# Performance work log

Measured on AMD Instinct MI355X. Metric: run time of the kernel, lower is better.

Reference implementation:

```python
import jax, jax.numpy as jnp
import numpy as np

THRESHOLD = 0.1
EPS = 1e-05


def setup_inputs() -> dict:
    key = jax.random.key(0)
    kx, kl, k1, k2 = jax.random.split(key, 4)
    B, S, D = 8, 4096, 1024
    Dh = max(2, D // 2)
    x = jax.random.normal(kx, (B, S, D), dtype=jnp.float32)
    # trailing (right) padding with random valid lengths in [S//2, S]
    lengths = jax.random.randint(kl, (B,), S // 2, S + 1)
    pad = jnp.arange(S)[None, :] >= lengths[:, None]  # [B, S] bool, True = padded
    W1 = jax.random.normal(k1, (D, Dh), dtype=jnp.float32) * (1.0 / np.sqrt(D))
    b1 = jnp.zeros((Dh,), dtype=jnp.float32)
    W2 = jax.random.normal(k2, (Dh, 1), dtype=jnp.float32) * (1.0 / np.sqrt(Dh))
    b2 = jnp.zeros((1,), dtype=jnp.float32)
    return {"x": x, "pad": pad, "W1": W1, "b1": b1, "W2": W2, "b2": b2}


def reference(x, pad, W1, b1, W2, b2):
    B, S, D = x.shape
    pos = jnp.arange(S)
    # number of valid (non-pad) tokens per batch; pad is trailing
    length = S - jnp.sum(pad, axis=1)  # [B]

    # tiny gate MLP: Linear -> ReLU -> Linear, squashed to (0, 1)
    h = jax.nn.relu(jnp.einsum('bsd,dh->bsh', x, W1) + b1)
    y = jnp.einsum('bsh,ho->bso', h, W2) + b2          # [B, S, 1]
    y = (1.0 + jnp.tanh(10.0 * y)) * 0.5

    # zero out gate values at padded positions (torch loop: y[i, n:] = 0)
    valid = pos[None, :] < length[:, None]             # [B, S]
    y = jnp.where(valid[..., None], y, 0.0)

    # lift so at least one token passes the threshold
    adjust = jnp.clip(EPS + THRESHOLD - jnp.max(y, axis=1), 0.0)  # [B, 1]
    y = y + adjust[:, None, :]                         # broadcast over seq

    u = x * y                                          # gated features [B, S, D]
    ys = y[..., 0]                                     # [B, S]
    u_mask = (ys > THRESHOLD) & (~pad)                 # tokens kept
    new_len = jnp.sum(u_mask, axis=1)                  # [B]

    # compact kept tokens to the front of each row (stable sort: kept first,
    # original order preserved) -- the mask-scatter v[v_mask] = u[u_mask]
    order = jnp.argsort(~u_mask, axis=1, stable=True)  # [B, S]
    v = jnp.take_along_axis(u, order[..., None], axis=1)
    v_mask = pos[None, :] < new_len[:, None]           # [B, S]
    v = jnp.where(v_mask[..., None], v, 0.0)
    v_pad = ~v_mask
    return v, v_pad
```

## Files before the change

### kernel.cpp

```cpp
#include <hip/hip_runtime.h>
#include <math.h>

#define NB 8
#define NS 4096
#define ND 1024
#define NDH 512
#define NTOK (NB*NS)
#define THRESH 0.1f
#define EPSV 1e-5f

using short8   = __attribute__((ext_vector_type(8)))  short;
using floatx16 = __attribute__((ext_vector_type(16))) float;
using floatv4  = __attribute__((ext_vector_type(4)))  float;

__device__ __forceinline__ unsigned short f32_to_bf16_rne(float f) {
  union { float f; unsigned u; } v; v.f = f;
  unsigned r = v.u + 0x7fffu + ((v.u >> 16) & 1u);
  return (unsigned short)(r >> 16);
}
__device__ __forceinline__ float bf16_to_f32(unsigned short h) {
  union { unsigned u; float f; } v; v.u = ((unsigned)h) << 16;
  return v.f;
}

__global__ __launch_bounds__(256)
void k0_prep(const float* __restrict__ W1, unsigned short* __restrict__ Wf,
             unsigned int* __restrict__ rowmax) {
  __shared__ float sw[16][513];
  const int t = threadIdx.x;
  const int k16 = blockIdx.x;
  if (k16 == 0 && t < NB) rowmax[t] = 0u;
#pragma unroll
  for (int i = 0; i < 8; ++i) {
    int flat = i * 256 + t;
    int r = flat >> 7, c4 = (flat & 127) << 2;
    *(float4*)&sw[r][c4] = *(const float4*)(W1 + (size_t)(k16 * 16 + r) * NDH + c4);
  }
  __syncthreads();
#pragma unroll
  for (int q = 0; q < 4; ++q) {
    int ss = q * 256 + t;
    int n32 = ss >> 6, lane = ss & 63;
    int n = n32 * 32 + (lane & 31);
    int kb = (lane >> 5) * 8;
    unsigned hi2[4], lo2[4];
#pragma unroll
    for (int j = 0; j < 4; ++j) {
      float w0 = sw[kb + 2 * j][n], w1 = sw[kb + 2 * j + 1][n];
      unsigned short h0 = f32_to_bf16_rne(w0), h1 = f32_to_bf16_rne(w1);
      unsigned short l0 = f32_to_bf16_rne(w0 - bf16_to_f32(h0));
      unsigned short l1 = f32_to_bf16_rne(w1 - bf16_to_f32(h1));
      hi2[j] = (unsigned)h0 | ((unsigned)h1 << 16);
      lo2[j] = (unsigned)l0 | ((unsigned)l1 << 16);
    }
    size_t cb = ((size_t)(n32 * 64 + k16) * 2) * 512 + (size_t)lane * 8;
    *(uint4*)(Wf + cb)       = make_uint4(hi2[0], hi2[1], hi2[2], hi2[3]);
    *(uint4*)(Wf + cb + 512) = make_uint4(lo2[0], lo2[1], lo2[2], lo2[3]);
  }
}

__global__ __launch_bounds__(256, 2)
void k1_gemm(const float* __restrict__ x, const unsigned short* __restrict__ Wf,
             const float* __restrict__ b1, const float* __restrict__ W2,
             const int* __restrict__ pad, const float* __restrict__ b2,
             float* __restrict__ ysq, unsigned int* __restrict__ rowmax) {
  __shared__ __align__(16) unsigned short sx[2][2][64 * 72];
  __shared__ float red[4][64];

  const int tid = threadIdx.x;
  const int wave = tid >> 6, lane = tid & 63;
  const int l31 = lane & 31, h5 = lane >> 5;
  const int tok0 = blockIdx.x * 64;

  floatx16 acc[2][4];
#pragma unroll
  for (int mt = 0; mt < 2; ++mt)
#pragma unroll
    for (int nt = 0; nt < 4; ++nt)
#pragma unroll
      for (int r = 0; r < 16; ++r) acc[mt][nt][r] = 0.f;

  const int sm = tid >> 2;
  const int sk = (tid & 3) * 16;
  const float* xrow = x + (size_t)(tok0 + sm) * ND + sk;

  const unsigned short* wb[4];
#pragma unroll
  for (int nt = 0; nt < 4; ++nt)
    wb[nt] = Wf + (((size_t)(wave * 4 + nt) * 64) * 2) * 512 + (size_t)lane * 8;

  auto stage_cvt = [&](int bf, const float4& a0, const float4& a1,
                       const float4& a2, const float4& a3) {
    float v16[16] = {a0.x, a0.y, a0.z, a0.w, a1.x, a1.y, a1.z, a1.w,
                     a2.x, a2.y, a2.z, a2.w, a3.x, a3.y, a3.z, a3.w};
    unsigned hp[8], lp[8];
#pragma unroll
    for (int j = 0; j < 8; ++j) {
      unsigned short h0 = f32_to_bf16_rne(v16[2 * j]);
      unsigned short h1 = f32_to_bf16_rne(v16[2 * j + 1]);
      unsigned short l0 = f32_to_bf16_rne(v16[2 * j] - bf16_to_f32(h0));
      unsigned short l1 = f32_to_bf16_rne(v16[2 * j + 1] - bf16_to_f32(h1));
      hp[j] = (unsigned)h0 | ((unsigned)h1 << 16);
      lp[j] = (unsigned)l0 | ((unsigned)l1 << 16);
    }
    *(uint4*)&sx[bf][0][sm * 72 + sk]     = make_uint4(hp[0], hp[1], hp[2], hp[3]);
    *(uint4*)&sx[bf][0][sm * 72 + sk + 8] = make_uint4(hp[4], hp[5], hp[6], hp[7]);
    *(uint4*)&sx[bf][1][sm * 72 + sk]     = make_uint4(lp[0], lp[1], lp[2], lp[3]);
    *(uint4*)&sx[bf][1][sm * 72 + sk + 8] = make_uint4(lp[4], lp[5], lp[6], lp[7]);
  };

  {
    float4 a0 = *(const float4*)xrow;
    float4 a1 = *(const float4*)(xrow + 4);
    float4 a2 = *(const float4*)(xrow + 8);
    float4 a3 = *(const float4*)(xrow + 12);
    stage_cvt(0, a0, a1, a2, a3);
  }

  for (int it = 0; it < 16; ++it) {
    const int p = it & 1;
    __syncthreads();
    float4 pa0, pa1, pa2, pa3;
    if (it < 15) {
      const float* xp = xrow + (it + 1) * 64;
      pa0 = *(const float4*)xp;
      pa1 = *(const float4*)(xp + 4);
      pa2 = *(const float4*)(xp + 8);
      pa3 = *(const float4*)(xp + 12);
    }
#pragma unroll
    for (int kh = 0; kh < 4; ++kh) {
      short8 bh[4], bl[4];
#pragma unroll
      for (int nt = 0; nt < 4; ++nt) {
        const unsigned short* q = wb[nt] + ((size_t)(4 * it + kh) * 2) * 512;
        bh[nt] = *(const short8*)(q);
        bl[nt] = *(const short8*)(q + 512);
      }
      short8 ah[2], al[2];
#pragma unroll
      for (int mt = 0; mt < 2; ++mt) {
        ah[mt] = *(const short8*)&sx[p][0][(mt * 32 + l31) * 72 + kh * 16 + h5 * 8];
        al[mt] = *(const short8*)&sx[p][1][(mt * 32 + l31) * 72 + kh * 16 + h5 * 8];
      }
#pragma unroll
      for (int nt = 0; nt < 4; ++nt)
#pragma unroll
        for (int mt = 0; mt < 2; ++mt)
          acc[mt][nt] = __builtin_amdgcn_mfma_f32_32x32x16_bf16(ah[mt], bh[nt], acc[mt][nt], 0, 0, 0);
#pragma unroll
      for (int nt = 0; nt < 4; ++nt)
#pragma unroll
        for (int mt = 0; mt < 2; ++mt)
          acc[mt][nt] = __builtin_amdgcn_mfma_f32_32x32x16_bf16(al[mt], bh[nt], acc[mt][nt], 0, 0, 0);
#pragma unroll
      for (int nt = 0; nt < 4; ++nt)
#pragma unroll
        for (int mt = 0; mt < 2; ++mt)
          acc[mt][nt] = __builtin_amdgcn_mfma_f32_32x32x16_bf16(ah[mt], bl[nt], acc[mt][nt], 0, 0, 0);
    }
    if (it < 15) stage_cvt(p ^ 1, pa0, pa1, pa2, pa3);
  }

  float b1v[4], w2v[4];
#pragma unroll
  for (int nt = 0; nt < 4; ++nt) {
    const int n = wave * 128 + nt * 32 + l31;
    b1v[nt] = b1[n];
    w2v[nt] = W2[n];
  }
#pragma unroll
  for (int mt = 0; mt < 2; ++mt) {
    float pr[16];
#pragma unroll
    for (int r = 0; r < 16; ++r) pr[r] = 0.f;
#pragma unroll
    for (int nt = 0; nt < 4; ++nt)
#pragma unroll
      for (int r = 0; r < 16; ++r)
        pr[r] += fmaxf(acc[mt][nt][r] + b1v[nt], 0.f) * w2v[nt];
#pragma unroll
    for (int m = 1; m <= 16; m <<= 1)
#pragma unroll
      for (int r = 0; r < 16; ++r) pr[r] += __shfl_xor(pr[r], m, 64);
    if (l31 == 0) {
#pragma unroll
      for (int r = 0; r < 16; ++r) {
        int row = (r & 3) + 8 * (r >> 2) + 4 * h5;
        red[wave][mt * 32 + row] = pr[r];
      }
    }
  }
  __syncthreads();
  if (tid < 64) {
    float s = red[0][tid] + red[1][tid] + red[2][tid] + red[3][tid];
    const int t = tok0 + tid;
    float yl = s + b2[0];
    float y = (1.f + tanhf(10.f * yl)) * 0.5f;
    if (pad[t]) y = 0.f;
    ysq[t] = y;
    float m = y;
#pragma unroll
    for (int o = 32; o >= 1; o >>= 1) m = fmaxf(m, __shfl_xor(m, o, 64));
    if (tid == 0) atomicMax(rowmax + (t >> 12), __float_as_uint(m));
  }
}

__global__ __launch_bounds__(1024)
void k2b(const float* __restrict__ ysq, const int* __restrict__ pad,
         const unsigned int* __restrict__ rowmax, float* __restrict__ gval,
         int* __restrict__ src_of_dest, int* __restrict__ new_len,
         float* __restrict__ vpad_out) {
  __shared__ int ssum[16];
  const int b = blockIdx.x, tid = threadIdx.x;
  const int lane = tid & 63, wv = tid >> 6;
  const int base = b * NS, s0 = tid * 4;
  const float adj = fmaxf(EPSV + THRESH - __uint_as_float(rowmax[b]), 0.f);

  float4 yq = *(const float4*)(ysq + base + s0);
  int4 pq = *(const int4*)(pad + base + s0);
  float yv[4] = {yq.x + adj, yq.y + adj, yq.z + adj, yq.w + adj};
  int pv[4] = {pq.x, pq.y, pq.z, pq.w};
  unsigned km = 0;
  int cnt = 0;
#pragma unroll
  for (int i = 0; i < 4; ++i) {
    bool keep = (yv[i] > THRESH) && !pv[i];
    if (keep) { km |= (1u << i); ++cnt; }
  }
  int inc = cnt;
#pragma unroll
  for (int o = 1; o < 64; o <<= 1) {
    int tmp = __shfl_up(inc, o, 64);
    if (lane >= o) inc += tmp;
  }
  if (lane == 63) ssum[wv] = inc;
  __syncthreads();
  int wpre = 0;
  int total = 0;
#pragma unroll
  for (int w = 0; w < 16; ++w) {
    int sv = ssum[w];
    if (w < wv) wpre += sv;
    total += sv;
  }
  int off = wpre + inc - cnt;
#pragma unroll
  for (int i = 0; i < 4; ++i) {
    int s = s0 + i;
    if ((km >> i) & 1u) {
      src_of_dest[base + off] = s;
      gval[base + off] = yv[i];
      ++off;
    }
    vpad_out[base + s] = (s >= total) ? 1.f : 0.f;
  }
  if (tid == 0) new_len[b] = total;
}

__global__ __launch_bounds__(256)
void k3_gather(const float* __restrict__ x, const float* __restrict__ gval,
               const int* __restrict__ src_of_dest, const int* __restrict__ new_len,
               float* __restrict__ v) {
  const int slot0 = blockIdx.x * 16;
  const int b = slot0 >> 12;
  const int nl = new_len[b];
  const int tid = threadIdx.x;
#pragma unroll
  for (int i = 0; i < 16; ++i) {
    const int slot = slot0 + i;
    const int dest = slot & (NS - 1);
    floatv4* vo = (floatv4*)(v + (size_t)slot * ND);
    floatv4 r;
    if (dest < nl) {
      const int src = src_of_dest[slot];
      const float g = gval[slot];
      floatv4 xv = ((const floatv4*)(x + ((size_t)b * NS + src) * ND))[tid];
      r = xv * g;
    } else {
      r = (floatv4)(0.f);
    }
    __builtin_nontemporal_store(r, vo + tid);
  }
}

extern "C" void kernel_launch(void* const* d_in, const int* in_sizes, int n_in,
                              void* d_out, int out_size, void* d_ws, size_t ws_size,
                              hipStream_t stream) {
  const float* x   = (const float*)d_in[0];
  const int*   pad = (const int*)d_in[1];
  const float* W1  = (const float*)d_in[2];
  const float* b1  = (const float*)d_in[3];
  const float* W2  = (const float*)d_in[4];
  const float* b2  = (const float*)d_in[5];

  float* v    = (float*)d_out;
  float* vpad = v + (size_t)NTOK * ND;

  unsigned short* Wf = (unsigned short*)(v + 24000000);

  float* ysq  = (float*)d_ws;
  float* gval = ysq + NTOK;
  int* src    = (int*)(gval + NTOK);
  int* nlen   = src + NTOK;
  unsigned int* rowmax = (unsigned int*)(nlen + NB);

  k0_prep<<<64, 256, 0, stream>>>(W1, Wf, rowmax);
  k1_gemm<<<NTOK / 64, 256, 0, stream>>>(x, Wf, b1, W2, pad, b2, ysq, rowmax);
  k2b<<<NB, 1024, 0, stream>>>(ysq, pad, rowmax, gval, src, nlen, vpad);
  k3_gather<<<NTOK / 16, 256, 0, stream>>>(x, gval, src, nlen, v);
}
```

Measured before the change: 315.4 us.

## Fuse per-row scan/compaction into GEMM tail via last-block-done counter

Removes the separate k2b kernel. Each GEMM block now bumps a per-batch-row atomic counter, and the last block to finish a row computes the row max, the threshold mask, the prefix scan and the scatter indices. This saves one kernel launch and the reads of the per-row atomicMax. In exchange the tail work runs on a single 256-thread block per row with 16 tokens per thread, and it relies on a threadfence/counter pattern for correctness.

```diff
diff --git a/kernel.cpp b/kernel.cpp
--- a/kernel.cpp
+++ b/kernel.cpp
@@ -25,11 +25,11 @@
 
 __global__ __launch_bounds__(256)
 void k0_prep(const float* __restrict__ W1, unsigned short* __restrict__ Wf,
-             unsigned int* __restrict__ rowmax) {
+             int* __restrict__ done_cnt) {
   __shared__ float sw[16][513];
   const int t = threadIdx.x;
   const int k16 = blockIdx.x;
-  if (k16 == 0 && t < NB) rowmax[t] = 0u;
+  if (k16 == 0 && t < NB) done_cnt[t] = 0;
 #pragma unroll
   for (int i = 0; i < 8; ++i) {
     int flat = i * 256 + t;
@@ -63,9 +63,14 @@
 void k1_gemm(const float* __restrict__ x, const unsigned short* __restrict__ Wf,
              const float* __restrict__ b1, const float* __restrict__ W2,
              const int* __restrict__ pad, const float* __restrict__ b2,
-             float* __restrict__ ysq, unsigned int* __restrict__ rowmax) {
+             float* __restrict__ ysq, int* __restrict__ done_cnt,
+             float* __restrict__ gval, int* __restrict__ src_of_dest,
+             int* __restrict__ new_len, float* __restrict__ vpad) {
   __shared__ __align__(16) unsigned short sx[2][2][64 * 72];
   __shared__ float red[4][64];
+  __shared__ float smax[4];
+  __shared__ int ssum[4];
+  __shared__ int sflag;
 
   const int tid = threadIdx.x;
   const int wave = tid >> 6, lane = tid & 63;
@@ -199,63 +204,63 @@
     float y = (1.f + tanhf(10.f * yl)) * 0.5f;
     if (pad[t]) y = 0.f;
     ysq[t] = y;
-    float m = y;
+  }
+  __threadfence();
+  __syncthreads();
+  const int brow = tok0 >> 12;
+  if (tid == 0) {
+    int prev = atomicAdd(&done_cnt[brow], 1);
+    sflag = (prev == 63) ? 1 : 0;
+  }
+  __syncthreads();
+  if (sflag) {
+    __threadfence();
+    const int base = brow * NS, s0 = tid * 16;
+    const int wv = wave;
+    float yv[16];
+#pragma unroll
+    for (int i = 0; i < 16; ++i) yv[i] = ysq[base + s0 + i];
+    float m = 0.f;
+#pragma unroll
+    for (int i = 0; i < 16; ++i) m = fmaxf(m, yv[i]);
 #pragma unroll
     for (int o = 32; o >= 1; o >>= 1) m = fmaxf(m, __shfl_xor(m, o, 64));
-    if (tid == 0) atomicMax(rowmax + (t >> 12), __float_as_uint(m));
-  }
-}
-
-__global__ __launch_bounds__(1024)
-void k2b(const float* __restrict__ ysq, const int* __restrict__ pad,
-         const unsigned int* __restrict__ rowmax, float* __restrict__ gval,
-         int* __restrict__ src_of_dest, int* __restrict__ new_len,
-         float* __restrict__ vpad_out) {
-  __shared__ int ssum[16];
-  const int b = blockIdx.x, tid = threadIdx.x;
-  const int lane = tid & 63, wv = tid >> 6;
-  const int base = b * NS, s0 = tid * 4;
-  const float adj = fmaxf(EPSV + THRESH - __uint_as_float(rowmax[b]), 0.f);
-
-  float4 yq = *(const float4*)(ysq + base + s0);
-  int4 pq = *(const int4*)(pad + base + s0);
-  float yv[4] = {yq.x + adj, yq.y + adj, yq.z + adj, yq.w + adj};
-  int pv[4] = {pq.x, pq.y, pq.z, pq.w};
-  unsigned km = 0;
-  int cnt = 0;
-#pragma unroll
-  for (int i = 0; i < 4; ++i) {
-    bool keep = (yv[i] > THRESH) && !pv[i];
-    if (keep) { km |= (1u << i); ++cnt; }
-  }
-  int inc = cnt;
-#pragma unroll
-  for (int o = 1; o < 64; o <<= 1) {
-    int tmp = __shfl_up(inc, o, 64);
-    if (lane >= o) inc += tmp;
-  }
-  if (lane == 63) ssum[wv] = inc;
-  __syncthreads();
-  int wpre = 0;
-  int total = 0;
-#pragma unroll
-  for (int w = 0; w < 16; ++w) {
-    int sv = ssum[w];
-    if (w < wv) wpre += sv;
-    total += sv;
-  }
-  int off = wpre + inc - cnt;
-#pragma unroll
-  for (int i = 0; i < 4; ++i) {
-    int s = s0 + i;
-    if ((km >> i) & 1u) {
-      src_of_dest[base + off] = s;
-      gval[base + off] = yv[i];
-      ++off;
-    }
-    vpad_out[base + s] = (s >= total) ? 1.f : 0.f;
-  }
-  if (tid == 0) new_len[b] = total;
+    if (lane == 0) smax[wv] = m;
+    __syncthreads();
+    const float rmax = fmaxf(fmaxf(smax[0], smax[1]), fmaxf(smax[2], smax[3]));
+    const float adj = fmaxf(EPSV + THRESH - rmax, 0.f);
+    unsigned km = 0;
+    int cnt = 0;
+#pragma unroll
+    for (int i = 0; i < 16; ++i) {
+      yv[i] += adj;
+      bool keep = (yv[i] > THRESH) && !pad[base + s0 + i];
+      if (keep) { km |= (1u << i); ++cnt; }
+    }
+    int inc = cnt;
+#pragma unroll
+    for (int o = 1; o < 64; o <<= 1) {
+      int tmp = __shfl_up(inc, o, 64);
+      if (lane >= o) inc += tmp;
+    }
+    if (lane == 63) ssum[wv] = inc;
+    __syncthreads();
+    int wpre = 0;
+    for (int w = 0; w < wv; ++w) wpre += ssum[w];
+    const int total = ssum[0] + ssum[1] + ssum[2] + ssum[3];
+    int off = wpre + inc - cnt;
+#pragma unroll
+    for (int i = 0; i < 16; ++i) {
+      int sdx = s0 + i;
+      if ((km >> i) & 1u) {
+        src_of_dest[base + off] = sdx;
+        gval[base + off] = yv[i];
+        ++off;
+      }
+      vpad[base + sdx] = (sdx >= total) ? 1.f : 0.f;
+    }
+    if (tid == 0) new_len[brow] = total;
+  }
 }
 
 __global__ __launch_bounds__(256)
@@ -303,10 +308,10 @@
   float* gval = ysq + NTOK;
   int* src    = (int*)(gval + NTOK);
   int* nlen   = src + NTOK;
-  unsigned int* rowmax = (unsigned int*)(nlen + NB);
-
-  k0_prep<<<64, 256, 0, stream>>>(W1, Wf, rowmax);
-  k1_gemm<<<NTOK / 64, 256, 0, stream>>>(x, Wf, b1, W2, pad, b2, ysq, rowmax);
-  k2b<<<NB, 1024, 0, stream>>>(ysq, pad, rowmax, gval, src, nlen, vpad);
+  int* dcnt   = nlen + NB;
+
+  k0_prep<<<64, 256, 0, stream>>>(W1, Wf, dcnt);
+  k1_gemm<<<NTOK / 64, 256, 0, stream>>>(x, Wf, b1, W2, pad, b2,
+                                         ysq, dcnt, gval, src, nlen, vpad);
   k3_gather<<<NTOK / 16, 256, 0, stream>>>(x, gval, src, nlen, v);
 }
```

Result: slower. 377.3 us (+19.6%).

## Split gate GEMM hidden dim across two blocks, combine with atomics

Applied to the files above, without the earlier changes.

Each k1_gemm block now computes only half of the 512 hidden columns for its 64 tokens. The grid doubles and launch bounds are raised to 4 blocks per CU, to get more parallelism and occupancy. Partial second-layer sums are combined into a buffer that k0 zeroes, using atomicAdd. The tanh, pad mask and row max move into k2b, which removes the global atomicMax rowmax. The cost is that every x tile is loaded and split to bf16 twice, doubling x traffic and conversion work in the GEMM.

```diff
diff --git a/kernel.cpp b/kernel.cpp
--- a/kernel.cpp
+++ b/kernel.cpp
@@ -25,11 +25,12 @@
 
 __global__ __launch_bounds__(256)
 void k0_prep(const float* __restrict__ W1, unsigned short* __restrict__ Wf,
-             unsigned int* __restrict__ rowmax) {
+             float* __restrict__ ysq) {
   __shared__ float sw[16][513];
   const int t = threadIdx.x;
   const int k16 = blockIdx.x;
-  if (k16 == 0 && t < NB) rowmax[t] = 0u;
+  ysq[k16 * 512 + t] = 0.f;
+  ysq[k16 * 512 + 256 + t] = 0.f;
 #pragma unroll
   for (int i = 0; i < 8; ++i) {
     int flat = i * 256 + t;
@@ -59,24 +60,24 @@
   }
 }
 
-__global__ __launch_bounds__(256, 2)
+__global__ __launch_bounds__(256, 4)
 void k1_gemm(const float* __restrict__ x, const unsigned short* __restrict__ Wf,
              const float* __restrict__ b1, const float* __restrict__ W2,
-             const int* __restrict__ pad, const float* __restrict__ b2,
-             float* __restrict__ ysq, unsigned int* __restrict__ rowmax) {
+             float* __restrict__ ysq) {
   __shared__ __align__(16) unsigned short sx[2][2][64 * 72];
   __shared__ float red[4][64];
 
   const int tid = threadIdx.x;
   const int wave = tid >> 6, lane = tid & 63;
   const int l31 = lane & 31, h5 = lane >> 5;
-  const int tok0 = blockIdx.x * 64;
-
-  floatx16 acc[2][4];
+  const int tok0 = (blockIdx.x >> 1) * 64;
+  const int nhalf = blockIdx.x & 1;
+
+  floatx16 acc[2][2];
 #pragma unroll
   for (int mt = 0; mt < 2; ++mt)
 #pragma unroll
-    for (int nt = 0; nt < 4; ++nt)
+    for (int nt = 0; nt < 2; ++nt)
 #pragma unroll
       for (int r = 0; r < 16; ++r) acc[mt][nt][r] = 0.f;
 
@@ -84,10 +85,12 @@
   const int sk = (tid & 3) * 16;
   const float* xrow = x + (size_t)(tok0 + sm) * ND + sk;
 
-  const unsigned short* wb[4];
-#pragma unroll
-  for (int nt = 0; nt < 4; ++nt)
-    wb[nt] = Wf + (((size_t)(wave * 4 + nt) * 64) * 2) * 512 + (size_t)lane * 8;
+  const unsigned short* wb[2];
+#pragma unroll
+  for (int nt = 0; nt < 2; ++nt) {
+    const int n32 = nhalf * 8 + wave * 2 + nt;
+    wb[nt] = Wf + (((size_t)n32 * 64) * 2) * 512 + (size_t)lane * 8;
+  }
 
   auto stage_cvt = [&](int bf, const float4& a0, const float4& a1,
                        const float4& a2, const float4& a3) {
@@ -130,9 +133,9 @@
     }
 #pragma unroll
     for (int kh = 0; kh < 4; ++kh) {
-      short8 bh[4], bl[4];
-#pragma unroll
-      for (int nt = 0; nt < 4; ++nt) {
+      short8 bh[2], bl[2];
+#pragma unroll
+      for (int nt = 0; nt < 2; ++nt) {
         const unsigned short* q = wb[nt] + ((size_t)(4 * it + kh) * 2) * 512;
         bh[nt] = *(const short8*)(q);
         bl[nt] = *(const short8*)(q + 512);
@@ -144,17 +147,17 @@
         al[mt] = *(const short8*)&sx[p][1][(mt * 32 + l31) * 72 + kh * 16 + h5 * 8];
       }
 #pragma unroll
-      for (int nt = 0; nt < 4; ++nt)
+      for (int nt = 0; nt < 2; ++nt)
 #pragma unroll
         for (int mt = 0; mt < 2; ++mt)
           acc[mt][nt] = __builtin_amdgcn_mfma_f32_32x32x16_bf16(ah[mt], bh[nt], acc[mt][nt], 0, 0, 0);
 #pragma unroll
-      for (int nt = 0; nt < 4; ++nt)
+      for (int nt = 0; nt < 2; ++nt)
 #pragma unroll
         for (int mt = 0; mt < 2; ++mt)
           acc[mt][nt] = __builtin_amdgcn_mfma_f32_32x32x16_bf16(al[mt], bh[nt], acc[mt][nt], 0, 0, 0);
 #pragma unroll
-      for (int nt = 0; nt < 4; ++nt)
+      for (int nt = 0; nt < 2; ++nt)
 #pragma unroll
         for (int mt = 0; mt < 2; ++mt)
           acc[mt][nt] = __builtin_amdgcn_mfma_f32_32x32x16_bf16(ah[mt], bl[nt], acc[mt][nt], 0, 0, 0);
@@ -162,10 +165,10 @@
     if (it < 15) stage_cvt(p ^ 1, pa0, pa1, pa2, pa3);
   }
 
-  float b1v[4], w2v[4];
-#pragma unroll
-  for (int nt = 0; nt < 4; ++nt) {
-    const int n = wave * 128 + nt * 32 + l31;
+  float b1v[2], w2v[2];
+#pragma unroll
+  for (int nt = 0; nt < 2; ++nt) {
+    const int n = nhalf * 256 + wave * 64 + nt * 32 + l31;
     b1v[nt] = b1[n];
     w2v[nt] = W2[n];
   }
@@ -175,7 +178,7 @@
 #pragma unroll
     for (int r = 0; r < 16; ++r) pr[r] = 0.f;
 #pragma unroll
-    for (int nt = 0; nt < 4; ++nt)
+    for (int nt = 0; nt < 2; ++nt)
 #pragma unroll
       for (int r = 0; r < 16; ++r)
         pr[r] += fmaxf(acc[mt][nt][r] + b1v[nt], 0.f) * w2v[nt];
@@ -194,37 +197,48 @@
   __syncthreads();
   if (tid < 64) {
     float s = red[0][tid] + red[1][tid] + red[2][tid] + red[3][tid];
-    const int t = tok0 + tid;
-    float yl = s + b2[0];
-    float y = (1.f + tanhf(10.f * yl)) * 0.5f;
-    if (pad[t]) y = 0.f;
-    ysq[t] = y;
-    float m = y;
-#pragma unroll
-    for (int o = 32; o >= 1; o >>= 1) m = fmaxf(m, __shfl_xor(m, o, 64));
-    if (tid == 0) atomicMax(rowmax + (t >> 12), __float_as_uint(m));
+    atomicAdd(ysq + tok0 + tid, s);
   }
 }
 
 __global__ __launch_bounds__(1024)
 void k2b(const float* __restrict__ ysq, const int* __restrict__ pad,
-         const unsigned int* __restrict__ rowmax, float* __restrict__ gval,
+         const float* __restrict__ b2, float* __restrict__ gval,
          int* __restrict__ src_of_dest, int* __restrict__ new_len,
          float* __restrict__ vpad_out) {
   __shared__ int ssum[16];
+  __shared__ float ssmax[16];
   const int b = blockIdx.x, tid = threadIdx.x;
   const int lane = tid & 63, wv = tid >> 6;
   const int base = b * NS, s0 = tid * 4;
-  const float adj = fmaxf(EPSV + THRESH - __uint_as_float(rowmax[b]), 0.f);
+  const float b2v = b2[0];
 
   float4 yq = *(const float4*)(ysq + base + s0);
   int4 pq = *(const int4*)(pad + base + s0);
-  float yv[4] = {yq.x + adj, yq.y + adj, yq.z + adj, yq.w + adj};
+  float yv[4] = {yq.x, yq.y, yq.z, yq.w};
   int pv[4] = {pq.x, pq.y, pq.z, pq.w};
+  float m4 = 0.f;
+#pragma unroll
+  for (int i = 0; i < 4; ++i) {
+    float y = (1.f + tanhf(10.f * (yv[i] + b2v))) * 0.5f;
+    if (pv[i]) y = 0.f;
+    yv[i] = y;
+    m4 = fmaxf(m4, y);
+  }
+#pragma unroll
+  for (int o = 32; o >= 1; o >>= 1) m4 = fmaxf(m4, __shfl_xor(m4, o, 64));
+  if (lane == 0) ssmax[wv] = m4;
+  __syncthreads();
+  float rmax = ssmax[0];
+#pragma unroll
+  for (int w = 1; w < 16; ++w) rmax = fmaxf(rmax, ssmax[w]);
+  const float adj = fmaxf(EPSV + THRESH - rmax, 0.f);
+
   unsigned km = 0;
   int cnt = 0;
 #pragma unroll
   for (int i = 0; i < 4; ++i) {
+    yv[i] += adj;
     bool keep = (yv[i] > THRESH) && !pv[i];
     if (keep) { km |= (1u << i); ++cnt; }
   }
@@ -303,10 +317,9 @@
   float* gval = ysq + NTOK;
   int* src    = (int*)(gval + NTOK);
   int* nlen   = src + NTOK;
-  unsigned int* rowmax = (unsigned int*)(nlen + NB);
-
-  k0_prep<<<64, 256, 0, stream>>>(W1, Wf, rowmax);
-  k1_gemm<<<NTOK / 64, 256, 0, stream>>>(x, Wf, b1, W2, pad, b2, ysq, rowmax);
-  k2b<<<NB, 1024, 0, stream>>>(ysq, pad, rowmax, gval, src, nlen, vpad);
+
+  k0_prep<<<64, 256, 0, stream>>>(W1, Wf, ysq);
+  k1_gemm<<<NTOK / 32, 256, 0, stream>>>(x, Wf, b1, W2, ysq);
+  k2b<<<NB, 1024, 0, stream>>>(ysq, pad, b2, gval, src, nlen, vpad);
   k3_gather<<<NTOK / 16, 256, 0, stream>>>(x, gval, src, nlen, v);
 }
```

Result: no change. 320.8 us (+1.7%).
